# Kernel tuning notes

Measured on AMD Instinct MI355X. Metric: run time of the kernel, lower is better.

Reference implementation:

```python
import jax, jax.numpy as jnp
import numpy as np

D_IN, N_HEADS, HEAD_DIM = 2048, 16, 128
SEQ, BATCH = 2048, 1
EPS = 1e-6


def rms_norm(x, scale, shift):
    # matches torch RMSNorm: computed in fp32, (1+scale)*x_norm + shift, cast back
    xf = x.astype(jnp.float32)
    rms = jnp.sqrt(jnp.mean(xf * xf, axis=-1, keepdims=True) + EPS)
    out = (xf / rms) * (1.0 + scale.astype(jnp.float32)) + shift.astype(jnp.float32)
    return out.astype(x.dtype)


def apply_rope(x, sin_t, cos_t):
    # x: [b, h, s, d]; sin/cos: [s, d]
    d = x.shape[-1]
    x1, x2 = x[..., : d // 2], x[..., d // 2 :]
    rot = jnp.concatenate([-x2, x1], axis=-1)
    return (x * cos_t[None, None] + rot * sin_t[None, None]).astype(x.dtype)


def setup_inputs() -> dict:
    key = jax.random.key(0)
    ks = jax.random.split(key, 8)
    x = jax.random.normal(ks[0], (BATCH, SEQ, D_IN), dtype=jnp.float32)
    # causal mask: True above the diagonal (positions to mask)
    mask = jnp.triu(jnp.ones((SEQ, SEQ), dtype=bool), k=1)
    # standard RoPE tables, shape [s, head_dim] (half-freqs tiled over both halves)
    inv_freq = 1.0 / (10000.0 ** (np.arange(0, HEAD_DIM, 2, dtype=np.float32) / HEAD_DIM))
    t = np.arange(SEQ, dtype=np.float32)
    ang = np.einsum('s,f->sf', t, inv_freq)          # [s, d/2]
    ang = np.concatenate([ang, ang], axis=-1)        # [s, d]
    sin_thetas = jnp.asarray(np.sin(ang))
    cos_thetas = jnp.asarray(np.cos(ang))
    d_out = N_HEADS * HEAD_DIM
    std = 0.02
    w_q = jax.random.normal(ks[1], (d_out, D_IN), dtype=jnp.float32) * std
    w_k = jax.random.normal(ks[2], (HEAD_DIM, D_IN), dtype=jnp.float32) * std
    w_v = jax.random.normal(ks[3], (HEAD_DIM, D_IN), dtype=jnp.float32) * std
    w_o = jax.random.normal(ks[4], (D_IN, d_out), dtype=jnp.float32) * std
    q_scale = jnp.zeros((HEAD_DIM,), jnp.float32)
    q_shift = jnp.zeros((HEAD_DIM,), jnp.float32)
    k_scale = jnp.zeros((HEAD_DIM,), jnp.float32)
    k_shift = jnp.zeros((HEAD_DIM,), jnp.float32)
    return dict(x=x, mask=mask, sin_thetas=sin_thetas, cos_thetas=cos_thetas,
                w_q=w_q, w_k=w_k, w_v=w_v, w_o=w_o,
                q_scale=q_scale, q_shift=q_shift, k_scale=k_scale, k_shift=k_shift)


def reference(x, mask, sin_thetas, cos_thetas, w_q, w_k, w_v, w_o,
              q_scale, q_shift, k_scale, k_shift):
    b, s, _ = x.shape
    scale = HEAD_DIM ** -0.5
    q = jnp.einsum('bsd,ed->bse', x, w_q).reshape(b, s, N_HEADS, HEAD_DIM)
    q = jnp.transpose(q, (0, 2, 1, 3))                 # [b, H, s, Dh]
    k = jnp.einsum('bsd,ed->bse', x, w_k)[:, None]     # [b, 1, s, Dh]
    v = jnp.einsum('bsd,ed->bse', x, w_v)[:, None]     # [b, 1, s, Dh]
    q = rms_norm(q, q_scale, q_shift)
    k = rms_norm(k, k_scale, k_shift)
    q = apply_rope(q, sin_thetas, cos_thetas)
    k = apply_rope(k, sin_thetas, cos_thetas)
    # MQA: broadcast single K/V head instead of repeat_interleave
    scores = jnp.einsum('bhqd,bokd->bhqk', q, k) * scale   # o==1 broadcast
    scores = jnp.where(mask[None, None], -jnp.inf, scores)
    w = jax.nn.softmax(scores, axis=-1)
    out = jnp.einsum('bhqk,bokd->bhqd', w, v)
    out = jnp.transpose(out, (0, 2, 1, 3)).reshape(b, s, N_HEADS * HEAD_DIM)
    return jnp.einsum('bse,de->bsd', out, w_o)
```

## Files before the change

kernel.cpp:

```cpp
#include <hip/hip_runtime.h>
#include <stdint.h>

#define SEQ 2048
#define DIN 2048
#define NH 16
#define HD 128

typedef __attribute__((ext_vector_type(8))) short bf16x8;
typedef __attribute__((ext_vector_type(4))) float f32x4;

__device__ __forceinline__ unsigned short f2bf(float f) {
    unsigned int u = __float_as_uint(f);
    u += 0x7fff + ((u >> 16) & 1);
    return (unsigned short)(u >> 16);
}

__device__ __forceinline__ float bf2f(unsigned short u) {
    return __uint_as_float(((unsigned int)u) << 16);
}

__device__ __forceinline__ void gload_lds16(const void* g, void* l) {
    __builtin_amdgcn_global_load_lds(
        (const __attribute__((address_space(1))) unsigned int*)g,
        (__attribute__((address_space(3))) unsigned int*)l,
        16, 0, 0);
}

__global__ void cast_all(const float* __restrict__ x,  const float* __restrict__ wq,
                         const float* __restrict__ wk, const float* __restrict__ wv,
                         const float* __restrict__ wo,
                         unsigned short* __restrict__ xb, unsigned short* __restrict__ wqk,
                         unsigned short* __restrict__ wvb, unsigned short* __restrict__ wob) {
    int i = blockIdx.x * blockDim.x + threadIdx.x;
    const float* src; unsigned short* dst; int off;
    if (i < 1048576)      { src = x;  dst = xb;            off = i; }
    else if (i < 2097152) { src = wq; dst = wqk;           off = i - 1048576; }
    else if (i < 2162688) { src = wk; dst = wqk + 4194304; off = i - 2097152; }
    else if (i < 2228224) { src = wv; dst = wvb;           off = i - 2162688; }
    else                  { src = wo; dst = wob;           off = i - 2228224; }
    float4 v = *reinterpret_cast<const float4*>(src + (size_t)off * 4);
    ushort4 o;
    o.x = f2bf(v.x); o.y = f2bf(v.y); o.z = f2bf(v.z); o.w = f2bf(v.w);
    *reinterpret_cast<ushort4*>(dst + (size_t)off * 4) = o;
}

template<int OUT_MODE>
__launch_bounds__(512)
__global__ void gemm_bt8(const unsigned short* __restrict__ A,
                         const unsigned short* __restrict__ B,
                         void* __restrict__ Cv, int M, int N, int K) {
    __shared__ __align__(16) unsigned short As[128 * 32];
    __shared__ __align__(16) unsigned short Bs[128 * 32];
    const int t = threadIdx.x;
    const int l = t & 63;
    const int w = t >> 6;
    const int wr = w >> 1, wc = w & 1;
    const int row0 = blockIdx.y * 128, col0 = blockIdx.x * 128;
    const int lr = l & 15, lk = (l >> 4) * 8;

    f32x4 acc[2][4] = {};

    const unsigned short* Ag = A + (size_t)(row0 + t / 4) * K + (t % 4) * 8;
    const unsigned short* Bg = B + (size_t)(col0 + t / 4) * K + (t % 4) * 8;

    for (int k0 = 0; k0 < K; k0 += 32) {
        gload_lds16(Ag + k0, &As[t * 8]);
        gload_lds16(Bg + k0, &Bs[t * 8]);
        __syncthreads();
        bf16x8 af[2], bfr[4];
#pragma unroll
        for (int m = 0; m < 2; ++m)
            af[m] = *reinterpret_cast<const bf16x8*>(&As[(wr * 32 + m * 16 + lr) * 32 + lk]);
#pragma unroll
        for (int n = 0; n < 4; ++n)
            bfr[n] = *reinterpret_cast<const bf16x8*>(&Bs[(wc * 64 + n * 16 + lr) * 32 + lk]);
#pragma unroll
        for (int m = 0; m < 2; ++m)
#pragma unroll
            for (int n = 0; n < 4; ++n)
                acc[m][n] = __builtin_amdgcn_mfma_f32_16x16x32_bf16(af[m], bfr[n], acc[m][n], 0, 0, 0);
        __syncthreads();
    }

#pragma unroll
    for (int m = 0; m < 2; ++m) {
        int row_b = row0 + wr * 32 + m * 16 + (l >> 4) * 4;
#pragma unroll
        for (int n = 0; n < 4; ++n) {
            int col = col0 + wc * 64 + n * 16 + lr;
#pragma unroll
            for (int jr = 0; jr < 4; ++jr) {
                int row = row_b + jr;
                if (OUT_MODE == 0)
                    ((float*)Cv)[(size_t)row * N + col] = acc[m][n][jr];
                else if (OUT_MODE == 1)
                    ((unsigned short*)Cv)[(size_t)row * N + col] = f2bf(acc[m][n][jr]);
                else
                    ((unsigned short*)Cv)[(size_t)col * M + row] = f2bf(acc[m][n][jr]);
            }
        }
    }
}

__global__ void norm_rope_all(const unsigned short* __restrict__ qk,
                              unsigned short* __restrict__ qout,
                              unsigned short* __restrict__ kout,
                              const float* __restrict__ sin_t, const float* __restrict__ cos_t,
                              const float* __restrict__ q_scale, const float* __restrict__ q_shift,
                              const float* __restrict__ k_scale, const float* __restrict__ k_shift) {
    int w = threadIdx.x >> 6, lane = threadIdx.x & 63;
    int vec = blockIdx.x * 4 + w;
    if (vec >= SEQ * NH + SEQ) return;
    const unsigned short* base;
    unsigned short* outp;
    const float *scale, *shift;
    int s;
    if (vec < SEQ * NH) {
        s = vec >> 4;
        int hh = vec & 15;
        base = qk + (size_t)s * 2176 + hh * HD;
        outp = qout + (size_t)vec * HD;
        scale = q_scale; shift = q_shift;
    } else {
        s = vec - SEQ * NH;
        base = qk + (size_t)s * 2176 + NH * HD;
        outp = kout + (size_t)s * HD;
        scale = k_scale; shift = k_shift;
    }
    float x1 = bf2f(base[lane]), x2 = bf2f(base[lane + 64]);
    float ss = x1 * x1 + x2 * x2;
#pragma unroll
    for (int off = 1; off < 64; off <<= 1) ss += __shfl_xor(ss, off, 64);
    float rinv = rsqrtf(ss * (1.0f / 128.0f) + 1e-6f);
    float xn1 = x1 * rinv * (1.0f + scale[lane]) + shift[lane];
    float xn2 = x2 * rinv * (1.0f + scale[lane + 64]) + shift[lane + 64];
    float c1 = cos_t[s * HD + lane], s1 = sin_t[s * HD + lane];
    float c2 = cos_t[s * HD + lane + 64], s2 = sin_t[s * HD + lane + 64];
    outp[lane]      = f2bf(xn1 * c1 - xn2 * s1);
    outp[lane + 64] = f2bf(xn2 * c2 + xn1 * s2);
}

__launch_bounds__(256)
__global__ void flash_attn3(const unsigned short* __restrict__ Q,
                            const unsigned short* __restrict__ Kb,
                            const unsigned short* __restrict__ Vtg,
                            unsigned short* __restrict__ O) {
    __shared__ __align__(16) unsigned short Ks[2][64 * 128];
    __shared__ __align__(16) unsigned short Vs[2][128 * 64];
    __shared__ __align__(16) unsigned short Pl[4][16 * 64];
    const int t = threadIdx.x, l = t & 63, w = t >> 6;
    const int bx = blockIdx.x;
    const int qt = (bx < 256) ? (31 - (bx >> 4)) : ((bx - 256) >> 4);
    const int h = bx & 15;
    const int lr = l & 15, g = l >> 4, lk = g * 8;
    const float sc = 0.08838834764831845f;

    auto stage = [&](int buf, int k0) {
#pragma unroll
        for (int i = 0; i < 4; ++i) {
            int c = w * 256 + i * 64 + l;
            int kr = c >> 4, kc = c & 15;
            gload_lds16(Kb + (size_t)(k0 + kr) * HD + ((kc ^ (kr & 7)) * 8),
                        &Ks[buf][c * 8]);
            int vd = c >> 3, vc = c & 7;
            gload_lds16(Vtg + (size_t)vd * SEQ + k0 + ((vc ^ (vd & 7)) * 8),
                        &Vs[buf][c * 8]);
        }
    };

    const int q0 = qt * 64;
    bf16x8 qf[4];
    const unsigned short* qbase = Q + (size_t)(q0 + w * 16 + lr) * (NH * HD) + h * HD + lk;
#pragma unroll
    for (int kf = 0; kf < 4; ++kf)
        qf[kf] = *reinterpret_cast<const bf16x8*>(qbase + kf * 32);

    f32x4 acc[8] = {};
    float mrow[4] = {-1e30f, -1e30f, -1e30f, -1e30f};
    float lrow[4] = {0.f, 0.f, 0.f, 0.f};
    const int nt = qt + 1;
    int buf = 0;
    stage(0, 0);
    __syncthreads();

    for (int kt = 0; kt < nt; ++kt) {
        if (kt + 1 < nt) stage(buf ^ 1, (kt + 1) * 64);

        f32x4 s4[4];
#pragma unroll
        for (int nf = 0; nf < 4; ++nf) {
            int row = nf * 16 + lr;
            f32x4 a = {};
#pragma unroll
            for (int kf = 0; kf < 4; ++kf) {
                bf16x8 kfrag = *reinterpret_cast<const bf16x8*>(
                    &Ks[buf][row * 128 + ((kf * 32 + lk) ^ ((row & 7) << 3))]);
                a = __builtin_amdgcn_mfma_f32_16x16x32_bf16(qf[kf], kfrag, a, 0, 0, 0);
            }
            s4[nf] = a;
        }

        float sv[4][4];
        const bool diag = (kt == qt);
#pragma unroll
        for (int jr = 0; jr < 4; ++jr)
#pragma unroll
            for (int nf = 0; nf < 4; ++nf) {
                float x = s4[nf][jr] * sc;
                if (diag && (nf * 16 + lr > w * 16 + g * 4 + jr)) x = -1e30f;
                sv[jr][nf] = x;
            }

        float mx[4];
#pragma unroll
        for (int jr = 0; jr < 4; ++jr) {
            float m2 = fmaxf(fmaxf(sv[jr][0], sv[jr][1]), fmaxf(sv[jr][2], sv[jr][3]));
            m2 = fmaxf(m2, __shfl_xor(m2, 1, 64));
            m2 = fmaxf(m2, __shfl_xor(m2, 2, 64));
            m2 = fmaxf(m2, __shfl_xor(m2, 4, 64));
            m2 = fmaxf(m2, __shfl_xor(m2, 8, 64));
            mx[jr] = m2;
        }
        int pred = (mx[0] - mrow[0] <= 8.f) && (mx[1] - mrow[1] <= 8.f) &&
                   (mx[2] - mrow[2] <= 8.f) && (mx[3] - mrow[3] <= 8.f);
        const bool skip = __all(pred);

#pragma unroll
        for (int jr = 0; jr < 4; ++jr) {
            float mnew = skip ? mrow[jr] : fmaxf(mrow[jr], mx[jr]);
            int row = g * 4 + jr;
            float ps = 0.f;
#pragma unroll
            for (int nf = 0; nf < 4; ++nf) {
                float p = __expf(sv[jr][nf] - mnew);
                ps += p;
                int col = nf * 16 + lr;
                Pl[w][row * 64 + (col ^ ((row & 12) << 2))] = f2bf(p);
            }
            ps += __shfl_xor(ps, 1, 64);
            ps += __shfl_xor(ps, 2, 64);
            ps += __shfl_xor(ps, 4, 64);
            ps += __shfl_xor(ps, 8, 64);
            if (!skip) {
                float corr = __expf(mrow[jr] - mnew);
                mrow[jr] = mnew;
                lrow[jr] = lrow[jr] * corr + ps;
#pragma unroll
                for (int nf = 0; nf < 8; ++nf) acc[nf][jr] *= corr;
            } else {
                lrow[jr] += ps;
            }
        }

        asm volatile("s_waitcnt lgkmcnt(0)" ::: "memory");
        __builtin_amdgcn_sched_barrier(0);

#pragma unroll
        for (int kf = 0; kf < 2; ++kf) {
            bf16x8 pf = *reinterpret_cast<const bf16x8*>(
                &Pl[w][lr * 64 + ((kf * 32 + lk) ^ ((lr & 12) << 2))]);
#pragma unroll
            for (int nf = 0; nf < 8; ++nf) {
                int d = nf * 16 + lr;
                bf16x8 vf = *reinterpret_cast<const bf16x8*>(
                    &Vs[buf][d * 64 + ((kf * 32 + lk) ^ ((d & 7) << 3))]);
                acc[nf] = __builtin_amdgcn_mfma_f32_16x16x32_bf16(pf, vf, acc[nf], 0, 0, 0);
            }
        }
        __syncthreads();
        buf ^= 1;
    }

#pragma unroll
    for (int jr = 0; jr < 4; ++jr) {
        float inv = 1.0f / lrow[jr];
        int row = q0 + w * 16 + g * 4 + jr;
#pragma unroll
        for (int nf = 0; nf < 8; ++nf) {
            int col = nf * 16 + lr;
            O[(size_t)row * (NH * HD) + h * HD + col] = f2bf(acc[nf][jr] * inv);
        }
    }
}

extern "C" void kernel_launch(void* const* d_in, const int* in_sizes, int n_in,
                              void* d_out, int out_size, void* d_ws, size_t ws_size,
                              hipStream_t stream) {
    const float* x      = (const float*)d_in[0];
    const float* sin_t  = (const float*)d_in[2];
    const float* cos_t  = (const float*)d_in[3];
    const float* w_q    = (const float*)d_in[4];
    const float* w_k    = (const float*)d_in[5];
    const float* w_v    = (const float*)d_in[6];
    const float* w_o    = (const float*)d_in[7];
    const float* q_scale = (const float*)d_in[8];
    const float* q_shift = (const float*)d_in[9];
    const float* k_scale = (const float*)d_in[10];
    const float* k_shift = (const float*)d_in[11];
    float* out = (float*)d_out;

    char* ws = (char*)d_ws;
    const size_t MB = 1u << 20;
    unsigned short* xb    = (unsigned short*)(ws);
    unsigned short* wqkb  = (unsigned short*)(ws + 8 * MB);
    unsigned short* wvb   = (unsigned short*)(ws + 16 * MB + 512 * 1024);
    unsigned short* wob   = (unsigned short*)(ws + 17 * MB);
    unsigned short* qkpre = (unsigned short*)(ws + 25 * MB);
    unsigned short* vtb   = (unsigned short*)(ws + 33 * MB + 512 * 1024);
    unsigned short* qb    = (unsigned short*)(ws + 34 * MB);
    unsigned short* kb    = (unsigned short*)(ws + 42 * MB);
    unsigned short* ab    = (unsigned short*)(ws + 42 * MB + 512 * 1024);

    cast_all<<<12800, 256, 0, stream>>>(x, w_q, w_k, w_v, w_o, xb, wqkb, wvb, wob);

    gemm_bt8<1><<<dim3(17, 16), 512, 0, stream>>>(xb, wqkb, qkpre, SEQ, NH * HD + HD, DIN);
    gemm_bt8<2><<<dim3(1, 16), 512, 0, stream>>>(xb, wvb, vtb, SEQ, HD, DIN);

    norm_rope_all<<<(SEQ * NH + SEQ) / 4, 256, 0, stream>>>(
        qkpre, qb, kb, sin_t, cos_t, q_scale, q_shift, k_scale, k_shift);

    flash_attn3<<<512, 256, 0, stream>>>(qb, kb, vtb, ab);

    gemm_bt8<0><<<dim3(16, 16), 512, 0, stream>>>(ab, wob, out, SEQ, NH * HD, DIN);
}
```

Measured before the change: 377.2 us.

## Fuse QKV projection into one GEMM and single-buffer V in flash attention

Concatenates the V weight after Q/K weights so a single 18-column-block GEMM produces Q/K pre-activations and the transposed V. This removes a separate one-block-wide V GEMM launch that ran at very low occupancy. In the attention kernel, V is now single-buffered and loaded within the same iteration, with launch_bounds raised to 2 blocks per CU, trading V prefetch overlap for lower LDS use and higher occupancy. It also swaps a waitcnt for a full __syncthreads before the PV stage.

After: 457.4 us. 21.3% more time.

```diff
diff --git a/kernel.cpp b/kernel.cpp
--- a/kernel.cpp
+++ b/kernel.cpp
@@ -29,26 +29,27 @@
 __global__ void cast_all(const float* __restrict__ x,  const float* __restrict__ wq,
                          const float* __restrict__ wk, const float* __restrict__ wv,
                          const float* __restrict__ wo,
-                         unsigned short* __restrict__ xb, unsigned short* __restrict__ wqk,
-                         unsigned short* __restrict__ wvb, unsigned short* __restrict__ wob) {
+                         unsigned short* __restrict__ xb, unsigned short* __restrict__ wqkv,
+                         unsigned short* __restrict__ wob) {
     int i = blockIdx.x * blockDim.x + threadIdx.x;
+    if (i >= 3276800) return;
     const float* src; unsigned short* dst; int off;
-    if (i < 1048576)      { src = x;  dst = xb;            off = i; }
-    else if (i < 2097152) { src = wq; dst = wqk;           off = i - 1048576; }
-    else if (i < 2162688) { src = wk; dst = wqk + 4194304; off = i - 2097152; }
-    else if (i < 2228224) { src = wv; dst = wvb;           off = i - 2162688; }
-    else                  { src = wo; dst = wob;           off = i - 2228224; }
+    if (i < 1048576)      { src = x;  dst = xb;             off = i; }
+    else if (i < 2097152) { src = wq; dst = wqkv;           off = i - 1048576; }
+    else if (i < 2162688) { src = wk; dst = wqkv + 4194304; off = i - 2097152; }
+    else if (i < 2228224) { src = wv; dst = wqkv + 4456448; off = i - 2162688; }
+    else                  { src = wo; dst = wob;            off = i - 2228224; }
     float4 v = *reinterpret_cast<const float4*>(src + (size_t)off * 4);
     ushort4 o;
     o.x = f2bf(v.x); o.y = f2bf(v.y); o.z = f2bf(v.z); o.w = f2bf(v.w);
     *reinterpret_cast<ushort4*>(dst + (size_t)off * 4) = o;
 }
 
-template<int OUT_MODE>
 __launch_bounds__(512)
-__global__ void gemm_bt8(const unsigned short* __restrict__ A,
+__global__ void gemm_qkv(const unsigned short* __restrict__ A,
                          const unsigned short* __restrict__ B,
-                         void* __restrict__ Cv, int M, int N, int K) {
+                         unsigned short* __restrict__ qkpre,
+                         unsigned short* __restrict__ vtb) {
     __shared__ __align__(16) unsigned short As[128 * 32];
     __shared__ __align__(16) unsigned short Bs[128 * 32];
     const int t = threadIdx.x;
@@ -57,9 +58,9 @@
     const int wr = w >> 1, wc = w & 1;
     const int row0 = blockIdx.y * 128, col0 = blockIdx.x * 128;
     const int lr = l & 15, lk = (l >> 4) * 8;
+    const int K = DIN;
 
     f32x4 acc[2][4] = {};
-
     const unsigned short* Ag = A + (size_t)(row0 + t / 4) * K + (t % 4) * 8;
     const unsigned short* Bg = B + (size_t)(col0 + t / 4) * K + (t % 4) * 8;
 
@@ -82,6 +83,7 @@
         __syncthreads();
     }
 
+    const bool isV = (blockIdx.x == 17);
 #pragma unroll
     for (int m = 0; m < 2; ++m) {
         int row_b = row0 + wr * 32 + m * 16 + (l >> 4) * 4;
@@ -91,13 +93,60 @@
 #pragma unroll
             for (int jr = 0; jr < 4; ++jr) {
                 int row = row_b + jr;
-                if (OUT_MODE == 0)
-                    ((float*)Cv)[(size_t)row * N + col] = acc[m][n][jr];
-                else if (OUT_MODE == 1)
-                    ((unsigned short*)Cv)[(size_t)row * N + col] = f2bf(acc[m][n][jr]);
+                if (isV)
+                    vtb[(size_t)(col - 2176) * SEQ + row] = f2bf(acc[m][n][jr]);
                 else
-                    ((unsigned short*)Cv)[(size_t)col * M + row] = f2bf(acc[m][n][jr]);
-            }
+                    qkpre[(size_t)row * 2176 + col] = f2bf(acc[m][n][jr]);
+            }
+        }
+    }
+}
+
+__launch_bounds__(512)
+__global__ void gemm_bt8(const unsigned short* __restrict__ A,
+                         const unsigned short* __restrict__ B,
+                         float* __restrict__ C, int M, int N, int K) {
+    __shared__ __align__(16) unsigned short As[128 * 32];
+    __shared__ __align__(16) unsigned short Bs[128 * 32];
+    const int t = threadIdx.x;
+    const int l = t & 63;
+    const int w = t >> 6;
+    const int wr = w >> 1, wc = w & 1;
+    const int row0 = blockIdx.y * 128, col0 = blockIdx.x * 128;
+    const int lr = l & 15, lk = (l >> 4) * 8;
+
+    f32x4 acc[2][4] = {};
+    const unsigned short* Ag = A + (size_t)(row0 + t / 4) * K + (t % 4) * 8;
+    const unsigned short* Bg = B + (size_t)(col0 + t / 4) * K + (t % 4) * 8;
+
+    for (int k0 = 0; k0 < K; k0 += 32) {
+        gload_lds16(Ag + k0, &As[t * 8]);
+        gload_lds16(Bg + k0, &Bs[t * 8]);
+        __syncthreads();
+        bf16x8 af[2], bfr[4];
+#pragma unroll
+        for (int m = 0; m < 2; ++m)
+            af[m] = *reinterpret_cast<const bf16x8*>(&As[(wr * 32 + m * 16 + lr) * 32 + lk]);
+#pragma unroll
+        for (int n = 0; n < 4; ++n)
+            bfr[n] = *reinterpret_cast<const bf16x8*>(&Bs[(wc * 64 + n * 16 + lr) * 32 + lk]);
+#pragma unroll
+        for (int m = 0; m < 2; ++m)
+#pragma unroll
+            for (int n = 0; n < 4; ++n)
+                acc[m][n] = __builtin_amdgcn_mfma_f32_16x16x32_bf16(af[m], bfr[n], acc[m][n], 0, 0, 0);
+        __syncthreads();
+    }
+
+#pragma unroll
+    for (int m = 0; m < 2; ++m) {
+        int row_b = row0 + wr * 32 + m * 16 + (l >> 4) * 4;
+#pragma unroll
+        for (int n = 0; n < 4; ++n) {
+            int col = col0 + wc * 64 + n * 16 + lr;
+#pragma unroll
+            for (int jr = 0; jr < 4; ++jr)
+                C[(size_t)(row_b + jr) * N + col] = acc[m][n][jr];
         }
     }
 }
@@ -140,13 +189,13 @@
     outp[lane + 64] = f2bf(xn2 * c2 + xn1 * s2);
 }
 
-__launch_bounds__(256)
-__global__ void flash_attn3(const unsigned short* __restrict__ Q,
+__launch_bounds__(256, 2)
+__global__ void flash_attn5(const unsigned short* __restrict__ Q,
                             const unsigned short* __restrict__ Kb,
                             const unsigned short* __restrict__ Vtg,
                             unsigned short* __restrict__ O) {
     __shared__ __align__(16) unsigned short Ks[2][64 * 128];
-    __shared__ __align__(16) unsigned short Vs[2][128 * 64];
+    __shared__ __align__(16) unsigned short Vs[128 * 64];
     __shared__ __align__(16) unsigned short Pl[4][16 * 64];
     const int t = threadIdx.x, l = t & 63, w = t >> 6;
     const int bx = blockIdx.x;
@@ -155,16 +204,22 @@
     const int lr = l & 15, g = l >> 4, lk = g * 8;
     const float sc = 0.08838834764831845f;
 
-    auto stage = [&](int buf, int k0) {
+    auto stageK = [&](int buf, int k0) {
 #pragma unroll
         for (int i = 0; i < 4; ++i) {
             int c = w * 256 + i * 64 + l;
             int kr = c >> 4, kc = c & 15;
             gload_lds16(Kb + (size_t)(k0 + kr) * HD + ((kc ^ (kr & 7)) * 8),
                         &Ks[buf][c * 8]);
+        }
+    };
+    auto stageV = [&](int k0) {
+#pragma unroll
+        for (int i = 0; i < 4; ++i) {
+            int c = w * 256 + i * 64 + l;
             int vd = c >> 3, vc = c & 7;
             gload_lds16(Vtg + (size_t)vd * SEQ + k0 + ((vc ^ (vd & 7)) * 8),
-                        &Vs[buf][c * 8]);
+                        &Vs[c * 8]);
         }
     };
 
@@ -180,11 +235,13 @@
     float lrow[4] = {0.f, 0.f, 0.f, 0.f};
     const int nt = qt + 1;
     int buf = 0;
-    stage(0, 0);
+    stageK(0, 0);
     __syncthreads();
 
     for (int kt = 0; kt < nt; ++kt) {
-        if (kt + 1 < nt) stage(buf ^ 1, (kt + 1) * 64);
+        const bool pf = (kt + 1 < nt);
+        stageV(kt * 64);
+        if (pf) stageK(buf ^ 1, (kt + 1) * 64);
 
         f32x4 s4[4];
 #pragma unroll
@@ -252,19 +309,18 @@
             }
         }
 
-        asm volatile("s_waitcnt lgkmcnt(0)" ::: "memory");
-        __builtin_amdgcn_sched_barrier(0);
+        __syncthreads();
 
 #pragma unroll
         for (int kf = 0; kf < 2; ++kf) {
-            bf16x8 pf = *reinterpret_cast<const bf16x8*>(
+            bf16x8 pfrag = *reinterpret_cast<const bf16x8*>(
                 &Pl[w][lr * 64 + ((kf * 32 + lk) ^ ((lr & 12) << 2))]);
 #pragma unroll
             for (int nf = 0; nf < 8; ++nf) {
                 int d = nf * 16 + lr;
                 bf16x8 vf = *reinterpret_cast<const bf16x8*>(
-                    &Vs[buf][d * 64 + ((kf * 32 + lk) ^ ((d & 7) << 3))]);
-                acc[nf] = __builtin_amdgcn_mfma_f32_16x16x32_bf16(pf, vf, acc[nf], 0, 0, 0);
+                    &Vs[d * 64 + ((kf * 32 + lk) ^ ((d & 7) << 3))]);
+                acc[nf] = __builtin_amdgcn_mfma_f32_16x16x32_bf16(pfrag, vf, acc[nf], 0, 0, 0);
             }
         }
         __syncthreads();
@@ -302,8 +358,7 @@
     char* ws = (char*)d_ws;
     const size_t MB = 1u << 20;
     unsigned short* xb    = (unsigned short*)(ws);
-    unsigned short* wqkb  = (unsigned short*)(ws + 8 * MB);
-    unsigned short* wvb   = (unsigned short*)(ws + 16 * MB + 512 * 1024);
+    unsigned short* wqkvb = (unsigned short*)(ws + 8 * MB);
     unsigned short* wob   = (unsigned short*)(ws + 17 * MB);
     unsigned short* qkpre = (unsigned short*)(ws + 25 * MB);
     unsigned short* vtb   = (unsigned short*)(ws + 33 * MB + 512 * 1024);
@@ -311,15 +366,14 @@
     unsigned short* kb    = (unsigned short*)(ws + 42 * MB);
     unsigned short* ab    = (unsigned short*)(ws + 42 * MB + 512 * 1024);
 
-    cast_all<<<12800, 256, 0, stream>>>(x, w_q, w_k, w_v, w_o, xb, wqkb, wvb, wob);
-
-    gemm_bt8<1><<<dim3(17, 16), 512, 0, stream>>>(xb, wqkb, qkpre, SEQ, NH * HD + HD, DIN);
-    gemm_bt8<2><<<dim3(1, 16), 512, 0, stream>>>(xb, wvb, vtb, SEQ, HD, DIN);
+    cast_all<<<12800, 256, 0, stream>>>(x, w_q, w_k, w_v, w_o, xb, wqkvb, wob);
+
+    gemm_qkv<<<dim3(18, 16), 512, 0, stream>>>(xb, wqkvb, qkpre, vtb);
 
     norm_rope_all<<<(SEQ * NH + SEQ) / 4, 256, 0, stream>>>(
         qkpre, qb, kb, sin_t, cos_t, q_scale, q_shift, k_scale, k_shift);
 
-    flash_attn3<<<512, 256, 0, stream>>>(qb, kb, vtb, ab);
-
-    gemm_bt8<0><<<dim3(16, 16), 512, 0, stream>>>(ab, wob, out, SEQ, NH * HD, DIN);
-}
+    flash_attn5<<<512, 256, 0, stream>>>(qb, kb, vtb, ab);
+
+    gemm_bt8<<<dim3(16, 16), 512, 0, stream>>>(ab, wob, out, SEQ, NH * HD, DIN);
+}
```
